# Kernel optimization log

Measured on AMD Instinct MI355X. Metric: run time of the kernel, lower is better.

Reference implementation:

```python
import jax, jax.numpy as jnp
import numpy as np

B, L, D, O = 4, 256, 512, 128

def setup_inputs() -> dict:
    key = jax.random.key(0)
    k1, k2, k3, k4, k5, k6 = jax.random.split(key, 6)
    return {
        "x1": jax.random.normal(k1, (B, L, D), jnp.float32),
        "x2": jax.random.normal(k2, (B, L, D), jnp.float32),
        "bw": jax.random.uniform(k3, (2,), jnp.float32),
        "W_bil": jax.random.normal(k4, (O, D + 1, D + 1), jnp.float32) * 0.02,
        "W_lin": jax.random.normal(k5, (2 * D, O), jnp.float32) * 0.02,
        "b_lin": jax.random.normal(k6, (O,), jnp.float32) * 0.02,
    }

def reference(x1, x2, bw, W_bil, W_lin, b_lin):
    bwn = jax.nn.softmax(bw)
    d1 = x1.shape[-1]
    # Bilinear with bias_x/bias_y: append ones column to x1 and x2.
    ones1 = jnp.ones((*x1.shape[:2], 1), x1.dtype)
    ones2 = jnp.ones((*x2.shape[:2], 1), x2.dtype)
    x1b = jnp.concatenate([x1, ones1], axis=-1)  # [B, L1, D+1]
    x2b = jnp.concatenate([x2, ones2], axis=-1)  # [B, L2, D+1]
    # einsum 'bxi,oij,byj->boxy' then permute(0,2,3,1) -> bxyo
    bilinear_logits = jnp.einsum('bxi,oij,byj->bxyo', x1b, W_bil, x2b)
    # linear over concat([x1 expanded, x2 expanded]) == split-weight broadcast sum
    lin1 = x1 @ W_lin[:d1]   # [B, L1, O]
    lin2 = x2 @ W_lin[d1:]   # [B, L2, O]
    linear_logits = lin1[:, :, None, :] + lin2[:, None, :, :] + b_lin  # [B, L1, L2, O]
    return bwn[0] * bilinear_logits + bwn[1] * linear_logits
```

## Files before the change

kernel.cpp:

```cpp
#include <hip/hip_runtime.h>


#define LL 256
#define DD 512
#define OO 128
#define BB 4
#define WB_OI 263169
#define WB_R512 262656

typedef __attribute__((ext_vector_type(8))) short  short8;
typedef __attribute__((ext_vector_type(8))) unsigned short us8;
typedef __attribute__((ext_vector_type(4))) unsigned short us4;
typedef __attribute__((ext_vector_type(4))) float  f32x4;

__device__ __forceinline__ unsigned short f2bf(float f) {
    unsigned int u = __builtin_bit_cast(unsigned int, f);
    u = (u + 0x7FFFu + ((u >> 16) & 1u)) >> 16;
    return (unsigned short)u;
}
__device__ __forceinline__ float bf2f(unsigned short s) {
    return __builtin_bit_cast(float, (unsigned int)s << 16);
}
__device__ __forceinline__ void load_lds16(const void* g, void* l) {
    __builtin_amdgcn_global_load_lds(
        (const __attribute__((address_space(1))) unsigned int*)g,
        (__attribute__((address_space(3))) unsigned int*)l, 16, 0, 0);
}

__global__ __launch_bounds__(256) void cast2_kernel(
    const float* __restrict__ x1, const float* __restrict__ x2,
    unsigned short* __restrict__ x1b, unsigned short* __restrict__ x2b)
{
    int i = blockIdx.x * 256 + threadIdx.x;
    const float* s; unsigned short* d; int j;
    if (i < 131072) { s = x1; d = x1b; j = i; }
    else            { s = x2; d = x2b; j = i - 131072; }
    float4 v = ((const float4*)s)[j];
    us4 u; u.x = f2bf(v.x); u.y = f2bf(v.y); u.z = f2bf(v.z); u.w = f2bf(v.w);
    *(us4*)(d + (size_t)j * 4) = u;
}

__global__ __launch_bounds__(256) void prepw_kernel(
    const float* __restrict__ Wb, const float* __restrict__ bw,
    unsigned short* __restrict__ Wb16)
{
    const int t = threadIdx.x;
    const int row = blockIdx.x * 4 + (t >> 6);
    const int o = row >> 9, i = row & 511;
    const int l = t & 63;
    const float e0 = __expf(bw[0]), e1 = __expf(bw[1]);
    const float bwn0 = e0 / (e0 + e1);
    const float* src = Wb + (size_t)o * WB_OI + (size_t)i * 513;
    unsigned short* dst = Wb16 + (size_t)row * 512;
    float v[8];
    #pragma unroll
    for (int e = 0; e < 8; ++e) v[e] = src[e * 64 + l];
    #pragma unroll
    for (int e = 0; e < 8; ++e) dst[e * 64 + l] = f2bf(bwn0 * v[e]);
}

__global__ __launch_bounds__(256) void prep512_kernel(
    const float* __restrict__ Wb, float* __restrict__ W512T)
{
    int idx = blockIdx.x * 256 + threadIdx.x;
    if (idx < 513 * 128) {
        const int o = idx & 127, j = idx >> 7;
        W512T[idx] = Wb[(size_t)o * WB_OI + WB_R512 + j];
    }
}

__global__ __launch_bounds__(128) void u512_kernel(
    const float* __restrict__ x2, const float* __restrict__ W512T,
    const float* __restrict__ W_lin, const float* __restrict__ b_lin,
    const float* __restrict__ bw, float* __restrict__ u512buf)
{
    __shared__ float xs[DD];
    const int by = blockIdx.x;
    const int o  = threadIdx.x;
    const float* xr = x2 + (size_t)by * DD;
    for (int j = o; j < DD; j += 128) xs[j] = xr[j];
    __syncthreads();
    float s1 = W512T[512 * 128 + o];
    float s2 = b_lin[o];
    #pragma unroll 4
    for (int j = 0; j < DD; ++j) {
        s1 += xs[j] * W512T[j * 128 + o];
        s2 += xs[j] * W_lin[(size_t)(DD + j) * OO + o];
    }
    const float e0 = __expf(bw[0]), e1 = __expf(bw[1]);
    const float bwn0 = e0 / (e0 + e1), bwn1 = e1 / (e0 + e1);
    u512buf[(size_t)by * OO + o] = bwn0 * s1 + bwn1 * s2;
}

__global__ __launch_bounds__(256) void passA_kernel(
    const unsigned short* __restrict__ x2b, const unsigned short* __restrict__ Wb16,
    const float* __restrict__ W_bil, const float* __restrict__ W_lin,
    const float* __restrict__ bw, unsigned short* __restrict__ Up)
{
    __shared__ __align__(16) char smem[65536];
    unsigned short* Cs  = (unsigned short*)smem;
    float* corr = (float*)(smem + 17408);

    const int t = threadIdx.x, w = t >> 6, l = t & 63;
    const int id  = blockIdx.x;
    const int lin = (id & 7) * 512 + (id >> 3);
    const int o   = lin >> 5;
    const int ib  = (lin & 3) * 128;
    const int yg  = ((lin >> 2) & 7) * 128;
    const int wy = w & 1, wx = w >> 1;

    f32x4 acc[4][4] = {};
    const unsigned short* Wo16 = Wb16 + (size_t)o * DD * DD;

    const int rb0 = w * 32;
    const int rr  = l >> 2;
    const int kof = ((l & 3) ^ ((l >> 3) & 3)) * 8;

#define STAGE_A(S, K0) do {                                                     \
    unsigned short* As_ = (unsigned short*)(smem + (S) * 16384);                \
    unsigned short* Bs_ = As_ + 4096;                                           \
    _Pragma("unroll")                                                           \
    for (int q = 0; q < 2; ++q) {                                               \
        const int rb = rb0 + q * 16, rrow = rb + rr, ko = (K0) + kof;           \
        load_lds16(x2b  + (size_t)(yg + rrow) * DD + ko, As_ + rb * 32);        \
        load_lds16(Wo16 + (size_t)(ib + rrow) * DD + ko, Bs_ + rb * 32);        \
    } } while (0)

    STAGE_A(0, 0); STAGE_A(1, 32); STAGE_A(2, 64);

    const int mrow = wy * 64 + (l & 15);
    const int ncol = wx * 64 + (l & 15);
    const int psel = ((l >> 4) ^ ((l >> 1) & 3)) * 8;

#define COMPUTE_T(S) do {                                                       \
    const unsigned short* As_ = (const unsigned short*)(smem + (S) * 16384);    \
    const unsigned short* Bs_ = As_ + 4096;                                     \
    short8 af[4], bfr[4];                                                       \
    _Pragma("unroll")                                                           \
    for (int mt = 0; mt < 4; ++mt) af[mt]  = *(const short8*)(As_ + (mrow + mt * 16) * 32 + psel); \
    _Pragma("unroll")                                                           \
    for (int nt = 0; nt < 4; ++nt) bfr[nt] = *(const short8*)(Bs_ + (ncol + nt * 16) * 32 + psel); \
    __builtin_amdgcn_s_setprio(1);                                              \
    _Pragma("unroll")                                                           \
    for (int mt = 0; mt < 4; ++mt)                                              \
        _Pragma("unroll")                                                       \
        for (int nt = 0; nt < 4; ++nt)                                          \
            acc[mt][nt] = __builtin_amdgcn_mfma_f32_16x16x32_bf16(af[mt], bfr[nt], acc[mt][nt], 0, 0, 0); \
    __builtin_amdgcn_s_setprio(0);                                              \
  } while (0)

    #pragma unroll
    for (int kt = 0; kt < 14; ++kt) {
        asm volatile("s_waitcnt vmcnt(8)" ::: "memory");
        __builtin_amdgcn_s_barrier();
        asm volatile("" ::: "memory");
        if (kt < 13) STAGE_A((kt + 3) & 3, (kt + 3) * 32);
        COMPUTE_T(kt & 3);
    }
    asm volatile("s_waitcnt vmcnt(4)" ::: "memory");
    __builtin_amdgcn_s_barrier();
    asm volatile("" ::: "memory");
    COMPUTE_T(2);
    asm volatile("s_waitcnt vmcnt(0)" ::: "memory");
    __builtin_amdgcn_s_barrier();
    asm volatile("" ::: "memory");
    COMPUTE_T(3);
#undef STAGE_A

    __syncthreads();
    const float e0 = __expf(bw[0]), e1 = __expf(bw[1]);
    const float bwn0 = e0 / (e0 + e1), bwn1 = e1 / (e0 + e1);
    if (t < 128) {
        const int ig = ib + t;
        corr[t] = bwn1 * W_lin[(size_t)ig * OO + o]
                + bwn0 * W_bil[(size_t)o * WB_OI + (size_t)ig * 513 + 512];
    }
    #pragma unroll
    for (int half = 0; half < 2; ++half) {
        if (wy == half) {
            #pragma unroll
            for (int mt = 0; mt < 4; ++mt) {
                const int yl = mt * 16 + ((l >> 4) << 2);
                #pragma unroll
                for (int nt = 0; nt < 4; ++nt) {
                    const int ic = wx * 64 + nt * 16 + (l & 15);
                    #pragma unroll
                    for (int r = 0; r < 4; ++r)
                        Cs[(yl + r) * 136 + ic] = f2bf(acc[mt][nt][r]);
                }
            }
        }
        __syncthreads();
        #pragma unroll
        for (int p = 0; p < 4; ++p) {
            const int yl = p * 16 + (t >> 4);
            const int i0 = (t & 15) * 8;
            short8 v = *(const short8*)(Cs + yl * 136 + i0);
            us8 uo;
            #pragma unroll
            for (int e = 0; e < 8; ++e)
                uo[e] = f2bf(bf2f((unsigned short)v[e]) + corr[i0 + e]);
            *(us8*)(Up + ((size_t)(yg + half * 64 + yl) * OO + o) * DD + ib + i0) = uo;
        }
        __syncthreads();
    }
}

__global__ __launch_bounds__(256) void passB_kernel(
    const unsigned short* __restrict__ x1b, const unsigned short* __restrict__ Up,
    const float* __restrict__ u512buf, float* __restrict__ out)
{
    __shared__ __align__(16) char smem[65536];

    const int t = threadIdx.x, w = t >> 6, l = t & 63;
    const int xb = blockIdx.x * 128;
    const int yg = blockIdx.y;
    const int bb = yg >> 8, y = yg & 255;
    const int wy = w & 1, wx = w >> 1;

    f32x4 acc[4][4] = {};

    const int rb0 = w * 32;
    const int rr  = l >> 2;
    const int kof = ((l & 3) ^ ((l >> 3) & 3)) * 8;

#define STAGE_B(S, K0) do {                                                          \
    unsigned short* As_ = (unsigned short*)(smem + (S) * 16384);                     \
    unsigned short* Bs_ = As_ + 4096;                                                \
    _Pragma("unroll")                                                                \
    for (int q = 0; q < 2; ++q) {                                                    \
        const int rb = rb0 + q * 16, rrow = rb + rr, ko = (K0) + kof;                \
        load_lds16(x1b + (size_t)(bb * LL + xb + rrow) * DD + ko, As_ + rb * 32);    \
        load_lds16(Up  + (size_t)(yg * OO + rrow) * DD + ko,      Bs_ + rb * 32);    \
    } } while (0)

    STAGE_B(0, 0); STAGE_B(1, 32); STAGE_B(2, 64);

    const int mrow = wy * 64 + (l & 15);
    const int ncol = wx * 64 + (l & 15);
    const int psel = ((l >> 4) ^ ((l >> 1) & 3)) * 8;

    #pragma unroll
    for (int kt = 0; kt < 14; ++kt) {
        asm volatile("s_waitcnt vmcnt(8)" ::: "memory");
        __builtin_amdgcn_s_barrier();
        asm volatile("" ::: "memory");
        if (kt < 13) STAGE_B((kt + 3) & 3, (kt + 3) * 32);
        COMPUTE_T(kt & 3);
    }
    asm volatile("s_waitcnt vmcnt(4)" ::: "memory");
    __builtin_amdgcn_s_barrier();
    asm volatile("" ::: "memory");
    COMPUTE_T(2);
    asm volatile("s_waitcnt vmcnt(0)" ::: "memory");
    __builtin_amdgcn_s_barrier();
    asm volatile("" ::: "memory");
    COMPUTE_T(3);
#undef STAGE_B

    #pragma unroll
    for (int mt = 0; mt < 4; ++mt) {
        const int xr = wy * 64 + mt * 16 + ((l >> 4) << 2);
        #pragma unroll
        for (int nt = 0; nt < 4; ++nt) {
            const int oc = wx * 64 + nt * 16 + (l & 15);
            const float c = u512buf[(size_t)yg * OO + oc];
            #pragma unroll
            for (int r = 0; r < 4; ++r)
                out[((size_t)(bb * LL + xb + xr + r) * LL + y) * OO + oc] = acc[mt][nt][r] + c;
        }
    }
}

extern "C" void kernel_launch(void* const* d_in, const int* in_sizes, int n_in,
                              void* d_out, int out_size, void* d_ws, size_t ws_size,
                              hipStream_t stream)
{
    const float* x1    = (const float*)d_in[0];
    const float* x2    = (const float*)d_in[1];
    const float* bw    = (const float*)d_in[2];
    const float* W_bil = (const float*)d_in[3];
    const float* W_lin = (const float*)d_in[4];
    const float* b_lin = (const float*)d_in[5];
    float* out = (float*)d_out;

    char* ws = (char*)d_ws;
    unsigned short* x1b16 = (unsigned short*)ws;
    unsigned short* x2b16 = (unsigned short*)(ws + (1u << 20));
    float*          u512b = (float*)(ws + (2u << 20));
    float*          W512T = (float*)(ws + (2u << 20) + (512u << 10));
    unsigned short* Wb16  = (unsigned short*)(ws + (3u << 20));
    unsigned short* Up    = (unsigned short*)(ws + (3u << 20) + ((size_t)128 * 512 * 512 * 2));

    cast2_kernel<<<1024, 256, 0, stream>>>(x1, x2, x1b16, x2b16);
    prepw_kernel<<<16384, 256, 0, stream>>>(W_bil, bw, Wb16);
    prep512_kernel<<<257, 256, 0, stream>>>(W_bil, W512T);
    u512_kernel<<<BB * LL, 128, 0, stream>>>(x2, W512T, W_lin, b_lin, bw, u512b);

    passA_kernel<<<4096, 256, 0, stream>>>(x2b16, Wb16, W_bil, W_lin, bw, Up);
    passB_kernel<<<dim3(2, BB * LL), 256, 0, stream>>>(x1b16, Up, u512b, out);
}
```

Baseline: 488.5 us.

## Switch GEMM pipelines to double-buffered 64-wide K tiles with fewer barriers

Both pass A and pass B GEMMs now stage K tiles 64 wide in two 32 KB LDS buffers with a new XOR swizzle, replacing the four-deep 32-wide ring. Each stage feeds two MFMA phases per barrier. The aim is to halve the barrier count and make the global-to-LDS loads larger and more contiguous. In exchange, prefetch depth drops to one tile and each step waits for vmcnt(0), which can expose more memory latency. The explicit __syncthreads before the epilogue is also removed, relying on the final loop barrier instead.

Result: no change. 484.8 us (-0.8%).

```diff
diff --git a/kernel.cpp b/kernel.cpp
--- a/kernel.cpp
+++ b/kernel.cpp
@@ -92,6 +92,30 @@
     u512buf[(size_t)by * OO + o] = bwn0 * s1 + bwn1 * s2;
 }
 
+#define PHASE(S, KS) do {                                                       \
+    const unsigned short* As_ = (const unsigned short*)(smem + (S) * 32768);    \
+    const unsigned short* Bs_ = As_ + 8192;                                     \
+    const int ck = (((KS) * 4 + lk) ^ lx7) * 8;                                 \
+    short8 af[4], bfr[4];                                                       \
+    _Pragma("unroll")                                                           \
+    for (int f = 0; f < 4; ++f) af[f]  = *(const short8*)(As_ + (mrow + f * 16) * 64 + ck); \
+    _Pragma("unroll")                                                           \
+    for (int f = 0; f < 4; ++f) bfr[f] = *(const short8*)(Bs_ + (ncol + f * 16) * 64 + ck); \
+    __builtin_amdgcn_s_setprio(1);                                              \
+    _Pragma("unroll")                                                           \
+    for (int mt = 0; mt < 4; ++mt)                                              \
+        _Pragma("unroll")                                                       \
+        for (int nt = 0; nt < 4; ++nt)                                          \
+            acc[mt][nt] = __builtin_amdgcn_mfma_f32_16x16x32_bf16(af[mt], bfr[nt], acc[mt][nt], 0, 0, 0); \
+    __builtin_amdgcn_s_setprio(0);                                              \
+  } while (0)
+
+#define WAIT_BAR(N) do {                                                        \
+    asm volatile("s_waitcnt vmcnt(" #N ")" ::: "memory");                       \
+    __builtin_amdgcn_s_barrier();                                               \
+    asm volatile("" ::: "memory");                                              \
+  } while (0)
+
 __global__ __launch_bounds__(256) void passA_kernel(
     const unsigned short* __restrict__ x2b, const unsigned short* __restrict__ Wb16,
     const float* __restrict__ W_bil, const float* __restrict__ W_lin,
@@ -112,62 +136,37 @@
     f32x4 acc[4][4] = {};
     const unsigned short* Wo16 = Wb16 + (size_t)o * DD * DD;
 
-    const int rb0 = w * 32;
-    const int rr  = l >> 2;
-    const int kof = ((l & 3) ^ ((l >> 3) & 3)) * 8;
-
-#define STAGE_A(S, K0) do {                                                     \
-    unsigned short* As_ = (unsigned short*)(smem + (S) * 16384);                \
-    unsigned short* Bs_ = As_ + 4096;                                           \
-    _Pragma("unroll")                                                           \
-    for (int q = 0; q < 2; ++q) {                                               \
-        const int rb = rb0 + q * 16, rrow = rb + rr, ko = (K0) + kof;           \
-        load_lds16(x2b  + (size_t)(yg + rrow) * DD + ko, As_ + rb * 32);        \
-        load_lds16(Wo16 + (size_t)(ib + rrow) * DD + ko, Bs_ + rb * 32);        \
+    const int rloc = t >> 3;
+    const int csw  = (t & 7) ^ (rloc & 7);
+
+#define STAGE_A(S, KT) do {                                                     \
+    unsigned short* As_ = (unsigned short*)(smem + (S) * 32768);                \
+    unsigned short* Bs_ = As_ + 8192;                                           \
+    const int gc = (KT) * 64 + csw * 8;                                         \
+    _Pragma("unroll")                                                           \
+    for (int q = 0; q < 4; ++q) {                                               \
+        const int row = q * 32 + rloc;                                          \
+        load_lds16(x2b  + (size_t)(yg + row) * DD + gc, As_ + q * 2048 + t * 8);\
+        load_lds16(Wo16 + (size_t)(ib + row) * DD + gc, Bs_ + q * 2048 + t * 8);\
     } } while (0)
-
-    STAGE_A(0, 0); STAGE_A(1, 32); STAGE_A(2, 64);
 
     const int mrow = wy * 64 + (l & 15);
     const int ncol = wx * 64 + (l & 15);
-    const int psel = ((l >> 4) ^ ((l >> 1) & 3)) * 8;
-
-#define COMPUTE_T(S) do {                                                       \
-    const unsigned short* As_ = (const unsigned short*)(smem + (S) * 16384);    \
-    const unsigned short* Bs_ = As_ + 4096;                                     \
-    short8 af[4], bfr[4];                                                       \
-    _Pragma("unroll")                                                           \
-    for (int mt = 0; mt < 4; ++mt) af[mt]  = *(const short8*)(As_ + (mrow + mt * 16) * 32 + psel); \
-    _Pragma("unroll")                                                           \
-    for (int nt = 0; nt < 4; ++nt) bfr[nt] = *(const short8*)(Bs_ + (ncol + nt * 16) * 32 + psel); \
-    __builtin_amdgcn_s_setprio(1);                                              \
-    _Pragma("unroll")                                                           \
-    for (int mt = 0; mt < 4; ++mt)                                              \
-        _Pragma("unroll")                                                       \
-        for (int nt = 0; nt < 4; ++nt)                                          \
-            acc[mt][nt] = __builtin_amdgcn_mfma_f32_16x16x32_bf16(af[mt], bfr[nt], acc[mt][nt], 0, 0, 0); \
-    __builtin_amdgcn_s_setprio(0);                                              \
-  } while (0)
-
-    #pragma unroll
-    for (int kt = 0; kt < 14; ++kt) {
-        asm volatile("s_waitcnt vmcnt(8)" ::: "memory");
-        __builtin_amdgcn_s_barrier();
-        asm volatile("" ::: "memory");
-        if (kt < 13) STAGE_A((kt + 3) & 3, (kt + 3) * 32);
-        COMPUTE_T(kt & 3);
-    }
-    asm volatile("s_waitcnt vmcnt(4)" ::: "memory");
-    __builtin_amdgcn_s_barrier();
-    asm volatile("" ::: "memory");
-    COMPUTE_T(2);
-    asm volatile("s_waitcnt vmcnt(0)" ::: "memory");
-    __builtin_amdgcn_s_barrier();
-    asm volatile("" ::: "memory");
-    COMPUTE_T(3);
+    const int lk   = l >> 4;
+    const int lx7  = l & 7;
+
+    STAGE_A(0, 0);
+    WAIT_BAR(0);
+    #pragma unroll
+    for (int kt = 0; kt < 8; ++kt) {
+        const int cur = kt & 1;
+        if (kt < 7) STAGE_A(cur ^ 1, kt + 1);
+        PHASE(cur, 0);
+        PHASE(cur, 1);
+        WAIT_BAR(0);
+    }
 #undef STAGE_A
 
-    __syncthreads();
     const float e0 = __expf(bw[0]), e1 = __expf(bw[1]);
     const float bwn0 = e0 / (e0 + e1), bwn1 = e1 / (e0 + e1);
     if (t < 128) {
@@ -220,42 +219,35 @@
 
     f32x4 acc[4][4] = {};
 
-    const int rb0 = w * 32;
-    const int rr  = l >> 2;
-    const int kof = ((l & 3) ^ ((l >> 3) & 3)) * 8;
-
-#define STAGE_B(S, K0) do {                                                          \
-    unsigned short* As_ = (unsigned short*)(smem + (S) * 16384);                     \
-    unsigned short* Bs_ = As_ + 4096;                                                \
+    const int rloc = t >> 3;
+    const int csw  = (t & 7) ^ (rloc & 7);
+
+#define STAGE_B(S, KT) do {                                                          \
+    unsigned short* As_ = (unsigned short*)(smem + (S) * 32768);                     \
+    unsigned short* Bs_ = As_ + 8192;                                                \
+    const int gc = (KT) * 64 + csw * 8;                                              \
     _Pragma("unroll")                                                                \
-    for (int q = 0; q < 2; ++q) {                                                    \
-        const int rb = rb0 + q * 16, rrow = rb + rr, ko = (K0) + kof;                \
-        load_lds16(x1b + (size_t)(bb * LL + xb + rrow) * DD + ko, As_ + rb * 32);    \
-        load_lds16(Up  + (size_t)(yg * OO + rrow) * DD + ko,      Bs_ + rb * 32);    \
+    for (int q = 0; q < 4; ++q) {                                                    \
+        const int row = q * 32 + rloc;                                               \
+        load_lds16(x1b + (size_t)(bb * LL + xb + row) * DD + gc, As_ + q * 2048 + t * 8); \
+        load_lds16(Up  + (size_t)(yg * OO + row) * DD + gc,      Bs_ + q * 2048 + t * 8); \
     } } while (0)
-
-    STAGE_B(0, 0); STAGE_B(1, 32); STAGE_B(2, 64);
 
     const int mrow = wy * 64 + (l & 15);
     const int ncol = wx * 64 + (l & 15);
-    const int psel = ((l >> 4) ^ ((l >> 1) & 3)) * 8;
-
-    #pragma unroll
-    for (int kt = 0; kt < 14; ++kt) {
-        asm volatile("s_waitcnt vmcnt(8)" ::: "memory");
-        __builtin_amdgcn_s_barrier();
-        asm volatile("" ::: "memory");
-        if (kt < 13) STAGE_B((kt + 3) & 3, (kt + 3) * 32);
-        COMPUTE_T(kt & 3);
-    }
-    asm volatile("s_waitcnt vmcnt(4)" ::: "memory");
-    __builtin_amdgcn_s_barrier();
-    asm volatile("" ::: "memory");
-    COMPUTE_T(2);
-    asm volatile("s_waitcnt vmcnt(0)" ::: "memory");
-    __builtin_amdgcn_s_barrier();
-    asm volatile("" ::: "memory");
-    COMPUTE_T(3);
+    const int lk   = l >> 4;
+    const int lx7  = l & 7;
+
+    STAGE_B(0, 0);
+    WAIT_BAR(0);
+    #pragma unroll
+    for (int kt = 0; kt < 8; ++kt) {
+        const int cur = kt & 1;
+        if (kt < 7) STAGE_B(cur ^ 1, kt + 1);
+        PHASE(cur, 0);
+        PHASE(cur, 1);
+        WAIT_BAR(0);
+    }
 #undef STAGE_B
 
     #pragma unroll
```
